# Performance work log

Hardware: AMD Instinct MI355X
Metric: run time of the kernel (lower is better)

## Reference

```python
import jax, jax.numpy as jnp
import numpy as np

B, N, C = 16, 577, 768
H, D = 12, 64
HID = 3072
EPS = 1e-5


def setup_inputs() -> dict:
    key = jax.random.key(0)
    ks = jax.random.split(key, 5)
    s = 0.02
    return {
        "x": jax.random.normal(ks[0], (B, N, C), jnp.float32),
        "w_qkv": jax.random.normal(ks[1], (C, 3 * C), jnp.float32) * s,
        "b_qkv": jnp.zeros((3 * C,), jnp.float32),
        "w_proj": jax.random.normal(ks[2], (C, C), jnp.float32) * s,
        "b_proj": jnp.zeros((C,), jnp.float32),
        "g1": jnp.ones((C,), jnp.float32),
        "be1": jnp.zeros((C,), jnp.float32),
        "g2": jnp.ones((C,), jnp.float32),
        "be2": jnp.zeros((C,), jnp.float32),
        "w1": jax.random.normal(ks[3], (C, HID), jnp.float32) * s,
        "b1": jnp.zeros((HID,), jnp.float32),
        "w2": jax.random.normal(ks[4], (HID, C), jnp.float32) * s,
        "b2": jnp.zeros((C,), jnp.float32),
    }


def _layernorm(x, g, b):
    mu = jnp.mean(x, axis=-1, keepdims=True)
    var = jnp.mean(jnp.square(x - mu), axis=-1, keepdims=True)
    return (x - mu) * jax.lax.rsqrt(var + EPS) * g + b


def reference(x, w_qkv, b_qkv, w_proj, b_proj, g1, be1, g2, be2, w1, b1, w2, b2):
    # --- pre-norm MHA ---
    xn = _layernorm(x, g1, be1)
    qkv = xn @ w_qkv + b_qkv                      # [B,N,3C]
    qkv = qkv.reshape(B, N, 3, H, D).transpose(2, 0, 3, 1, 4)  # [3,B,H,N,D]
    q, k, v = qkv[0], qkv[1], qkv[2]
    scale = 1.0 / jnp.sqrt(jnp.float32(D))
    scores = jnp.einsum("bhnd,bhmd->bhnm", q, k) * scale
    attn_weights = jax.nn.softmax(scores, axis=-1)  # [B,H,N,N]
    ctx = jnp.einsum("bhnm,bhmd->bhnd", attn_weights, v)
    ctx = ctx.transpose(0, 2, 1, 3).reshape(B, N, C)
    attn_out = ctx @ w_proj + b_proj
    x = x + attn_out
    # --- MLP (exact GELU, matching nn.GELU default) ---
    h = _layernorm(x, g2, be2) @ w1 + b1
    h = jax.nn.gelu(h, approximate=False)
    x = x + (h @ w2 + b2)
    return x, attn_weights
```

## Files before the change

### kernel.cpp

```cpp
#include <hip/hip_runtime.h>
#include <hip/hip_bf16.h>
#include <cmath>

constexpr int B_ = 16, N_ = 577, C_ = 768, H_ = 12, D_ = 64, HID_ = 3072;
constexpr int ROWS_ = B_ * N_;
constexpr int BH_ = B_ * H_;
constexpr int KVT_ = 10;
constexpr int QBLK_ = 10;

typedef __attribute__((ext_vector_type(8))) __bf16 bf16x8;
typedef __attribute__((ext_vector_type(4))) float f32x4;
typedef __attribute__((ext_vector_type(4), aligned(4))) float f32x4u;

#define DEVI __device__ __forceinline__

DEVI unsigned short f2bf(float f) {
  unsigned u = __float_as_uint(f);
  return (unsigned short)((u + 0x7fffu + ((u >> 16) & 1u)) >> 16);
}
DEVI float bf2f(unsigned short u) { return __uint_as_float(((unsigned)u) << 16); }

DEVI void gload16(const void* src, void* dst) {
  __builtin_amdgcn_global_load_lds(
      (const __attribute__((address_space(1))) char*)src,
      (__attribute__((address_space(3))) char*)dst, 16, 0, 0);
}
#define VMCNT0 asm volatile("s_waitcnt vmcnt(0)" ::: "memory")
#define VMW(n) asm volatile("s_waitcnt vmcnt(" #n ")" ::: "memory")
#define FENCE asm volatile("" ::: "memory")
#define RAWBAR do { FENCE; __builtin_amdgcn_s_barrier(); FENCE; } while (0)

__global__ __launch_bounds__(256) void cvtT_kernel(const float* __restrict__ in,
                                                   unsigned short* __restrict__ out,
                                                   int K, int N) {
  __shared__ float t[64][65];
  int n0 = blockIdx.x * 64, k0 = blockIdx.y * 64;
  int tx = threadIdx.x & 63, ty = threadIdx.x >> 6;
#pragma unroll
  for (int r = 0; r < 16; r++) {
    int kr = ty * 16 + r;
    t[kr][tx] = in[(long)(k0 + kr) * N + n0 + tx];
  }
  __syncthreads();
#pragma unroll
  for (int r = 0; r < 16; r++) {
    int nr = ty * 16 + r;
    out[(long)(n0 + nr) * K + k0 + tx] = f2bf(t[tx][nr]);
  }
}

__global__ __launch_bounds__(256) void ln_kernel(const float* __restrict__ x,
                                                 const float* __restrict__ g,
                                                 const float* __restrict__ be,
                                                 unsigned short* __restrict__ out) {
  int row = blockIdx.x;
  const float* xr = x + (long)row * C_;
  float v[3];
  float s = 0.f, s2 = 0.f;
#pragma unroll
  for (int j = 0; j < 3; j++) {
    int i = threadIdx.x + j * 256;
    v[j] = xr[i];
    s += v[j];
    s2 += v[j] * v[j];
  }
#pragma unroll
  for (int o = 32; o > 0; o >>= 1) {
    s += __shfl_down(s, o);
    s2 += __shfl_down(s2, o);
  }
  __shared__ float sh[8];
  int w = threadIdx.x >> 6;
  if ((threadIdx.x & 63) == 0) { sh[w] = s; sh[4 + w] = s2; }
  __syncthreads();
  s = sh[0] + sh[1] + sh[2] + sh[3];
  s2 = sh[4] + sh[5] + sh[6] + sh[7];
  float mu = s * (1.f / C_);
  float var = s2 * (1.f / C_) - mu * mu;
  float rs = rsqrtf(var + 1e-5f);
#pragma unroll
  for (int j = 0; j < 3; j++) {
    int i = threadIdx.x + j * 256;
    out[(long)row * C_ + i] = f2bf((v[j] - mu) * rs * g[i] + be[i]);
  }
}

__global__ __launch_bounds__(256) void attn_kernel(
    const unsigned short* __restrict__ qg,
    const unsigned short* __restrict__ kg,
    const unsigned short* __restrict__ vt,
    float* __restrict__ attn,
    unsigned short* __restrict__ ctx) {
  __shared__ unsigned short Ks[3][64][64];
  __shared__ unsigned short Vs[3][64][64];
  __shared__ unsigned short Ps[4][16][72];
  const int wgid = (blockIdx.x & 7) * (BH_ * QBLK_ / 8) + (blockIdx.x >> 3);
  const int bh = wgid / QBLK_, qb = wgid % QBLK_;
  const int b = bh / H_, h = bh % H_;
  const int tid = threadIdx.x, wave = tid >> 6, lane = tid & 63;
  const int l15 = lane & 15, l4 = lane >> 4;
  const int q0w = qb * 64 + wave * 16;

  const unsigned short* Qh = qg + (long)bh * N_ * D_;
  const char* Kb = (const char*)(kg + (long)bh * N_ * D_);
  const char* Vb = (const char*)(vt + (long)bh * D_ * N_);

  int qrc = q0w + l15; if (qrc >= N_) qrc = N_ - 1;
  bf16x8 qa0 = *(const bf16x8*)(Qh + (long)qrc * D_ + l4 * 8);
  bf16x8 qa1 = *(const bf16x8*)(Qh + (long)qrc * D_ + 32 + l4 * 8);

  auto srcAddr = [&](const char* g0, long rstride, int i) -> const char* {
    int off = i * 4096 + tid * 16;
    int row = off >> 7, colD = off & 127;
    return g0 + (long)row * rstride + (colD ^ ((row & 7) << 4));
  };
  auto stageK = [&](int bu, int kt) {
    const char* g0 = Kb + (long)kt * 8192;
#pragma unroll
    for (int i = 0; i < 2; i++)
      gload16(srcAddr(g0, 128, i), ((char*)Ks) + bu * 8192 + i * 4096 + wave * 1024);
  };
  auto stageV = [&](int bu, int kt) {
    const char* g0 = Vb + (long)kt * 128;
#pragma unroll
    for (int i = 0; i < 2; i++)
      gload16(srcAddr(g0, (long)N_ * 2, i), ((char*)Vs) + bu * 8192 + i * 4096 + wave * 1024);
  };
  auto rdK = [&](int bu, int row, int colb) -> bf16x8 {
    return *(const bf16x8*)(((const char*)Ks) + bu * 8192 + row * 128 +
                            (colb ^ ((row & 7) << 4)));
  };
  auto rdV = [&](int bu, int row, int colb) -> bf16x8 {
    return *(const bf16x8*)(((const char*)Vs) + bu * 8192 + row * 128 +
                            (colb ^ ((row & 7) << 4)));
  };
  auto computeS = [&](int bu, int kv0, f32x4 (&s)[4]) {
#pragma unroll
    for (int nf = 0; nf < 4; nf++) {
      int row = nf * 16 + l15;
      bf16x8 k0v = rdK(bu, row, l4 * 16);
      bf16x8 k1v = rdK(bu, row, 64 + l4 * 16);
      f32x4 z = {0.f, 0.f, 0.f, 0.f};
      z = __builtin_amdgcn_mfma_f32_16x16x32_bf16(qa0, k0v, z, 0, 0, 0);
      z = __builtin_amdgcn_mfma_f32_16x16x32_bf16(qa1, k1v, z, 0, 0, 0);
      if (kv0 + row >= N_) z = f32x4{-1e30f, -1e30f, -1e30f, -1e30f};
      s[nf] = z;
    }
  };

  float m_ln[4], l_ln[4];
#pragma unroll
  for (int r = 0; r < 4; r++) { m_ln[r] = -1e30f; l_ln[r] = 0.f; }

  stageK(0, 0); stageK(1, 1);
#pragma unroll
  for (int kt = 0; kt < KVT_; kt++) {
    const int bu = kt % 3;
    if (kt < KVT_ - 1) { VMW(2); } else { VMW(0); }
    RAWBAR;
    if (kt + 2 < KVT_) stageK((kt + 2) % 3, kt + 2);
    f32x4 s[4];
    computeS(bu, kt * 64, s);
#pragma unroll
    for (int r = 0; r < 4; r++) {
      float t0 = fmaxf(fmaxf(s[0][r], s[1][r]), fmaxf(s[2][r], s[3][r]));
      float mn = fmaxf(m_ln[r], t0);
      float sc = __expf(m_ln[r] - mn);
      l_ln[r] = l_ln[r] * sc + __expf(s[0][r] - mn) + __expf(s[1][r] - mn) +
                __expf(s[2][r] - mn) + __expf(s[3][r] - mn);
      m_ln[r] = mn;
    }
  }

  RAWBAR;
  stageK(0, 0); stageV(0, 0); stageK(1, 1); stageV(1, 1);

  float m_run[4], inv_l[4];
#pragma unroll
  for (int r = 0; r < 4; r++) {
    float m = m_ln[r];
#pragma unroll
    for (int o = 1; o < 16; o <<= 1) m = fmaxf(m, __shfl_xor(m, o));
    float li = l_ln[r] * __expf(m_ln[r] - m);
#pragma unroll
    for (int o = 1; o < 16; o <<= 1) li += __shfl_xor(li, o);
    m_run[r] = m;
    inv_l[r] = 1.f / li;
  }

  f32x4 cacc[4];
#pragma unroll
  for (int nf = 0; nf < 4; nf++) cacc[nf] = f32x4{0.f, 0.f, 0.f, 0.f};

#pragma unroll
  for (int kt = 0; kt < KVT_; kt++) {
    const int bu = kt % 3;
    const int kv0 = kt * 64;
    if (kt == 0) { VMW(4); }
    else if (kt == 1) { VMW(8); }
    else if (kt < KVT_ - 1) { VMW(12); }
    else { VMW(8); }
    RAWBAR;
    if (kt + 2 < KVT_) { stageK((kt + 2) % 3, kt + 2); stageV((kt + 2) % 3, kt + 2); }
    f32x4 s[4];
    computeS(bu, kv0, s);
#pragma unroll
    for (int nf = 0; nf < 4; nf++)
#pragma unroll
      for (int r = 0; r < 4; r++) {
        float p = __expf(s[nf][r] - m_run[r]) * inv_l[r];
        Ps[wave][l4 * 4 + r][nf * 16 + l15] = f2bf(p);
      }
    if (kt < KVT_ - 1) {
      int prow = lane >> 4;
      int c0 = (lane & 15) * 4;
#pragma unroll
      for (int rg = 0; rg < 4; rg++) {
        int row = rg * 4 + prow;
        int qv = q0w + row;
        if (qv < N_) {
          ushort4 pb = *(const ushort4*)&Ps[wave][row][c0];
          f32x4u f;
          f[0] = bf2f(pb.x); f[1] = bf2f(pb.y); f[2] = bf2f(pb.z); f[3] = bf2f(pb.w);
          __builtin_nontemporal_store(
              f, (f32x4u*)(attn + ((long)bh * N_ + qv) * N_ + kv0 + c0));
        }
      }
    } else {
      if ((lane & 15) == 0) {
        int prow = lane >> 4;
#pragma unroll
        for (int rg = 0; rg < 4; rg++) {
          int row = rg * 4 + prow;
          int qv = q0w + row;
          if (qv < N_)
            __builtin_nontemporal_store(bf2f(Ps[wave][row][0]),
                                        attn + ((long)bh * N_ + qv) * N_ + 576);
        }
      }
    }
#pragma unroll
    for (int ks = 0; ks < 2; ks++) {
      bf16x8 pa = *(const bf16x8*)&Ps[wave][l15][ks * 32 + l4 * 8];
#pragma unroll
      for (int nf = 0; nf < 4; nf++) {
        bf16x8 vb = rdV(bu, nf * 16 + l15, ks * 64 + l4 * 16);
        cacc[nf] = __builtin_amdgcn_mfma_f32_16x16x32_bf16(pa, vb, cacc[nf], 0, 0, 0);
      }
    }
  }

#pragma unroll
  for (int nf = 0; nf < 4; nf++)
#pragma unroll
    for (int r = 0; r < 4; r++) {
      int qv = q0w + l4 * 4 + r;
      if (qv >= N_) continue;
      int d = nf * 16 + l15;
      ctx[((long)b * N_ + qv) * C_ + h * D_ + d] = f2bf(cacc[nf][r]);
    }
}

template <int EPI>
__global__ __launch_bounds__(256) void gemm128(
    const unsigned short* __restrict__ A,
    const unsigned short* __restrict__ BT,
    int M, int K, int Nc,
    void* __restrict__ outp, const float* __restrict__ bias,
    const float* __restrict__ resid) {
  __shared__ unsigned short As[2][128][64];
  __shared__ unsigned short Bs[2][128][64];
  const int tid = threadIdx.x, wave = tid >> 6, lane = tid & 63;
  const int l15 = lane & 15, l4 = lane >> 4;
  const long m0 = (long)blockIdx.y * 128, n0 = (long)blockIdx.x * 128;
  const int wr = (wave >> 1) * 64, wc = (wave & 1) * 64;

  f32x4 acc[4][4];
#pragma unroll
  for (int i = 0; i < 4; i++)
#pragma unroll
    for (int j = 0; j < 4; j++) acc[i][j] = f32x4{0.f, 0.f, 0.f, 0.f};

  auto stageA = [&](int buf, int t) {
#pragma unroll
    for (int i = 0; i < 4; i++) {
      int off = i * 4096 + tid * 16;
      int row = off >> 7, colD = off & 127;
      long gr = m0 + row; if (gr >= M) gr = M - 1;
      const char* src = (const char*)A + (gr * (long)K + (long)t * 64) * 2 +
                        (colD ^ ((row & 7) << 4));
      char* dst = ((char*)As) + buf * 16384 + i * 4096 + wave * 1024;
      gload16(src, dst);
    }
  };
  auto stageB = [&](int buf, int t) {
#pragma unroll
    for (int i = 0; i < 4; i++) {
      int off = i * 4096 + tid * 16;
      int row = off >> 7, colD = off & 127;
      const char* src = (const char*)BT + ((n0 + row) * (long)K + (long)t * 64) * 2 +
                        (colD ^ ((row & 7) << 4));
      char* dst = ((char*)Bs) + buf * 16384 + i * 4096 + wave * 1024;
      gload16(src, dst);
    }
  };

  const int nt = K / 64;
  stageA(0, 0); stageB(0, 0);
  VMCNT0; __syncthreads();
  int buf = 0;
  for (int t = 0; t < nt; t++) {
    if (t + 1 < nt) { stageA(buf ^ 1, t + 1); stageB(buf ^ 1, t + 1); }
    bf16x8 af[4][2], bfr[4][2];
#pragma unroll
    for (int mf = 0; mf < 4; mf++)
#pragma unroll
      for (int kk = 0; kk < 2; kk++) {
        int row = wr + mf * 16 + l15, colb = kk * 64 + l4 * 16;
        af[mf][kk] = *(const bf16x8*)(((const char*)As) + buf * 16384 + row * 128 +
                                      (colb ^ ((row & 7) << 4)));
      }
#pragma unroll
    for (int nf = 0; nf < 4; nf++)
#pragma unroll
      for (int kk = 0; kk < 2; kk++) {
        int row = wc + nf * 16 + l15, colb = kk * 64 + l4 * 16;
        bfr[nf][kk] = *(const bf16x8*)(((const char*)Bs) + buf * 16384 + row * 128 +
                                       (colb ^ ((row & 7) << 4)));
      }
#pragma unroll
    for (int kk = 0; kk < 2; kk++)
#pragma unroll
      for (int mf = 0; mf < 4; mf++)
#pragma unroll
        for (int nf = 0; nf < 4; nf++)
          acc[mf][nf] =
              __builtin_amdgcn_mfma_f32_16x16x32_bf16(af[mf][kk], bfr[nf][kk], acc[mf][nf], 0, 0, 0);
    VMCNT0; __syncthreads();
    buf ^= 1;
  }

#pragma unroll
  for (int mf = 0; mf < 4; mf++)
#pragma unroll
    for (int nf = 0; nf < 4; nf++)
#pragma unroll
      for (int r = 0; r < 4; r++) {
        long row = m0 + wr + mf * 16 + l4 * 4 + r;
        long col = n0 + wc + nf * 16 + l15;
        if (row >= M) continue;
        float v = acc[mf][nf][r];
        if constexpr (EPI == 3 || EPI == 5) {
          float* o = (float*)outp;
          long idx = row * (long)Nc + col;
          o[idx] = v + bias[col] + resid[idx];
        } else if constexpr (EPI == 4) {
          v += bias[col];
          float ge = 0.5f * v * (1.f + erff(v * 0.70710678118654752f));
          ((unsigned short*)outp)[row * (long)Nc + col] = f2bf(ge);
        }
      }
}

template <int EPI>
__global__ __launch_bounds__(512, 2) void gemm256(
    const unsigned short* __restrict__ A,
    const unsigned short* __restrict__ BT,
    int M, int K, int Nc,
    void* __restrict__ outp, const float* __restrict__ bias,
    const float* __restrict__ resid) {
  __shared__ unsigned short smem[2][2][2][128][64];
  const int tid = threadIdx.x, wave = tid >> 6, lane = tid & 63;
  const int l15 = lane & 15, l4 = lane >> 4;
  const int wm = wave >> 2, wn = wave & 3;

  const int nbx = gridDim.x;
  const int nwg = nbx * gridDim.y;
  int orig = blockIdx.y * nbx + blockIdx.x;
  int qq = nwg >> 3, r8 = nwg & 7;
  int xcd = orig & 7, idx = orig >> 3;
  int wg = (xcd < r8 ? xcd * (qq + 1) : r8 * (qq + 1) + (xcd - r8) * qq) + idx;
  const long m0 = (long)(wg / nbx) * 256;
  const long n0 = (long)(wg % nbx) * 256;

  f32x4 acc[2][2][4][2];
#pragma unroll
  for (int a = 0; a < 2; a++)
#pragma unroll
    for (int b = 0; b < 2; b++)
#pragma unroll
      for (int m = 0; m < 4; m++)
#pragma unroll
        for (int n = 0; n < 2; n++) acc[a][b][m][n] = f32x4{0.f, 0.f, 0.f, 0.f};

  auto stage = [&](int d, int op, int half, int t) {
#pragma unroll
    for (int it = 0; it < 2; it++) {
      int off = it * 8192 + tid * 16;
      int lrow = off >> 7, colb = off & 127;
      long grow;
      if (op == 0) {
        grow = m0 + half * 128 + lrow;
        if (grow >= M) grow = M - 1;
      } else {
        grow = n0 + half * 128 + lrow;
      }
      const unsigned short* gp = (op == 0) ? A : BT;
      const char* src = (const char*)(gp + grow * (long)K + (long)t * 64) +
                        (colb ^ ((lrow & 7) << 4));
      char* dst = ((char*)smem) + (((d * 2 + op) * 2 + half) * 16384) + off;
      gload16(src, dst);
    }
  };
  auto rdfrag = [&](int d, int op, int half, int lr, int kk) -> bf16x8 {
    const char* p = ((const char*)smem) + (((d * 2 + op) * 2 + half) * 16384) + lr * 128 +
                    ((kk * 64 + l4 * 16) ^ ((lr & 7) << 4));
    return *(const bf16x8*)p;
  };

  bf16x8 av[4][2];

#define PHASE(d, qm, qn, STAGECODE, VMCODE)                                              \
  {                                                                                      \
    if constexpr (qn == 0) {                                                             \
      _Pragma("unroll") for (int m = 0; m < 4; m++)                                      \
          _Pragma("unroll") for (int kk = 0; kk < 2; kk++)                               \
              av[m][kk] = rdfrag(d, 0, qm, wm * 64 + m * 16 + l15, kk);                  \
    }                                                                                    \
    bf16x8 bv[2][2];                                                                     \
    _Pragma("unroll") for (int n = 0; n < 2; n++)                                        \
        _Pragma("unroll") for (int kk = 0; kk < 2; kk++)                                 \
            bv[n][kk] = rdfrag(d, 1, qn, wn * 32 + n * 16 + l15, kk);                    \
    STAGECODE;                                                                           \
    VMCODE;                                                                              \
    RAWBAR;                                                                              \
    __builtin_amdgcn_s_setprio(1);                                                       \
    _Pragma("unroll") for (int kk = 0; kk < 2; kk++)                                     \
        _Pragma("unroll") for (int m = 0; m < 4; m++)                                    \
            _Pragma("unroll") for (int n = 0; n < 2; n++)                                \
                acc[qm][qn][m][n] = __builtin_amdgcn_mfma_f32_16x16x32_bf16(             \
                    av[m][kk], bv[n][kk], acc[qm][qn][m][n], 0, 0, 0);                   \
    __builtin_amdgcn_s_setprio(0);                                                       \
    RAWBAR;                                                                              \
  }

  const int nt = K / 64, ni = nt / 2;
  stage(0, 0, 0, 0); stage(0, 0, 1, 0); stage(0, 1, 0, 0); stage(0, 1, 1, 0);
  stage(1, 0, 0, 1); stage(1, 0, 1, 1); stage(1, 1, 0, 1); stage(1, 1, 1, 1);
  asm volatile("s_waitcnt vmcnt(8)" ::: "memory");
  RAWBAR;

  for (int i = 0; i < ni; i++) {
    const int t1 = 2 * i + 1, t2 = 2 * i + 2, t3 = 2 * i + 3;
    PHASE(0, 0, 0, { if (i > 0) stage(1, 0, 1, t1); }, {});
    PHASE(0, 0, 1, { if (i > 0) stage(1, 1, 1, t1); }, {});
    PHASE(0, 1, 0, { if (t2 < nt) stage(0, 0, 0, t2); }, {});
    PHASE(0, 1, 1, { if (t2 < nt) stage(0, 1, 0, t2); },
          { if (t2 < nt) { asm volatile("s_waitcnt vmcnt(4)" ::: "memory"); }
            else { asm volatile("s_waitcnt vmcnt(0)" ::: "memory"); } });
    PHASE(1, 0, 0, { if (t2 < nt) stage(0, 0, 1, t2); }, {});
    PHASE(1, 0, 1, { if (t2 < nt) stage(0, 1, 1, t2); }, {});
    PHASE(1, 1, 0, { if (t3 < nt) stage(1, 0, 0, t3); }, {});
    PHASE(1, 1, 1, { if (t3 < nt) stage(1, 1, 0, t3); },
          { if (t3 < nt) { asm volatile("s_waitcnt vmcnt(4)" ::: "memory"); }
            else { asm volatile("s_waitcnt vmcnt(0)" ::: "memory"); } });
  }
#undef PHASE

#pragma unroll
  for (int qm = 0; qm < 2; qm++)
#pragma unroll
    for (int qn = 0; qn < 2; qn++)
#pragma unroll
      for (int m = 0; m < 4; m++)
#pragma unroll
        for (int n = 0; n < 2; n++)
#pragma unroll
          for (int r = 0; r < 4; r++) {
            long row = m0 + qm * 128 + wm * 64 + m * 16 + l4 * 4 + r;
            long col = n0 + qn * 128 + wn * 32 + n * 16 + l15;
            if (row >= M) continue;
            float v = acc[qm][qn][m][n][r];
            if constexpr (EPI == 0) {
              v += bias[col];
              int which = (int)col / C_;
              int rem = (int)col % C_;
              int hh = rem >> 6, d = rem & 63;
              int bb = (int)row / N_, nn = (int)row % N_;
              if (which == 0) v *= 0.125f;
              unsigned short* o = (unsigned short*)outp;
              long base = (long)which * ((long)BH_ * N_ * D_);
              long oidx;
              if (which < 2)
                oidx = base + (((long)(bb * H_ + hh)) * N_ + nn) * D_ + d;
              else
                oidx = base + (((long)(bb * H_ + hh)) * D_ + d) * N_ + nn;
              o[oidx] = f2bf(v);
            } else if constexpr (EPI == 4) {
              v += bias[col];
              float ge = 0.5f * v * (1.f + erff(v * 0.70710678118654752f));
              ((unsigned short*)outp)[row * (long)Nc + col] = f2bf(ge);
            } else {
              float* o = (float*)outp;
              long oidx = row * (long)Nc + col;
              o[oidx] = v + bias[col] + resid[oidx];
            }
          }
}

extern "C" void kernel_launch(void* const* d_in, const int* in_sizes, int n_in,
                              void* d_out, int out_size, void* d_ws, size_t ws_size,
                              hipStream_t stream) {
  const float* x = (const float*)d_in[0];
  const float* w_qkv = (const float*)d_in[1];
  const float* b_qkv = (const float*)d_in[2];
  const float* w_proj = (const float*)d_in[3];
  const float* b_proj = (const float*)d_in[4];
  const float* g1 = (const float*)d_in[5];
  const float* be1 = (const float*)d_in[6];
  const float* g2 = (const float*)d_in[7];
  const float* be2 = (const float*)d_in[8];
  const float* w1 = (const float*)d_in[9];
  const float* b1 = (const float*)d_in[10];
  const float* w2 = (const float*)d_in[11];
  const float* b2 = (const float*)d_in[12];

  char* ws = (char*)d_ws;
  const size_t SZ_TOK_BF = (size_t)ROWS_ * C_ * 2;
  unsigned short* xn = (unsigned short*)(ws);
  unsigned short* q = (unsigned short*)(ws + SZ_TOK_BF);
  unsigned short* v = (unsigned short*)(ws + 3 * SZ_TOK_BF);
  unsigned short* ctx = (unsigned short*)(ws + 4 * SZ_TOK_BF);
  unsigned short* hbuf = q;
  float* x1 = (float*)(ws + 5 * SZ_TOK_BF);
  unsigned short* wqkvT = (unsigned short*)(ws + 5 * SZ_TOK_BF + (size_t)ROWS_ * C_ * 4);
  unsigned short* wprojT = wqkvT + (size_t)C_ * 3 * C_;
  unsigned short* w1T = wprojT + (size_t)C_ * C_;
  unsigned short* w2T = w1T + (size_t)C_ * HID_;

  float* out_x = (float*)d_out;
  float* attn = out_x + (size_t)ROWS_ * C_;

  cvtT_kernel<<<dim3(3 * C_ / 64, C_ / 64), 256, 0, stream>>>(w_qkv, wqkvT, C_, 3 * C_);
  cvtT_kernel<<<dim3(C_ / 64, C_ / 64), 256, 0, stream>>>(w_proj, wprojT, C_, C_);
  cvtT_kernel<<<dim3(HID_ / 64, C_ / 64), 256, 0, stream>>>(w1, w1T, C_, HID_);
  cvtT_kernel<<<dim3(C_ / 64, HID_ / 64), 256, 0, stream>>>(w2, w2T, HID_, C_);

  ln_kernel<<<ROWS_, 256, 0, stream>>>(x, g1, be1, xn);

  {
    dim3 g(3 * C_ / 256, (ROWS_ + 255) / 256);
    gemm256<0><<<g, 512, 0, stream>>>(xn, wqkvT, ROWS_, C_, 3 * C_, q, b_qkv, nullptr);
  }
  attn_kernel<<<BH_ * QBLK_, 256, 0, stream>>>(q, q + (size_t)BH_ * N_ * D_, v, attn, ctx);
  {
    dim3 g(C_ / 128, (ROWS_ + 127) / 128);
    gemm128<3><<<g, 256, 0, stream>>>(ctx, wprojT, ROWS_, C_, C_, x1, b_proj, x);
  }
  ln_kernel<<<ROWS_, 256, 0, stream>>>(x1, g2, be2, xn);
  {
    dim3 g(HID_ / 256, (ROWS_ + 255) / 256);
    gemm256<4><<<g, 512, 0, stream>>>(xn, w1T, ROWS_, C_, HID_, hbuf, b1, nullptr);
  }
  {
    dim3 g(C_ / 128, (ROWS_ + 127) / 128);
    gemm128<5><<<g, 256, 0, stream>>>(hbuf, w2T, ROWS_, HID_, C_, out_x, b2, x1);
  }
}
```

Before: 484.2 us.

## Transpose attention score MFMA so each lane owns a query row, store probabilities directly

The attention kernel swaps the MFMA operand order so each lane holds scores for a single query row across key columns. Row max and sum then become per-lane scalars with two cross-lane shuffles instead of per-row arrays reduced over 16 lanes. Attention weights are written straight from registers as fp32 instead of round-tripping through shared memory as bf16, and out-of-range query rows are redirected to a dump buffer rather than branched around. K/V staging drops from triple to double buffering with full vmcnt waits, which shrinks LDS use but risks exposing load latency.

New measurement: 491.2 us. About the same (+1.4%).

```diff
diff --git a/kernel.cpp b/kernel.cpp
--- a/kernel.cpp
+++ b/kernel.cpp
@@ -18,7 +18,6 @@
   unsigned u = __float_as_uint(f);
   return (unsigned short)((u + 0x7fffu + ((u >> 16) & 1u)) >> 16);
 }
-DEVI float bf2f(unsigned short u) { return __uint_as_float(((unsigned)u) << 16); }
 
 DEVI void gload16(const void* src, void* dst) {
   __builtin_amdgcn_global_load_lds(
@@ -90,10 +89,11 @@
     const unsigned short* __restrict__ kg,
     const unsigned short* __restrict__ vt,
     float* __restrict__ attn,
-    unsigned short* __restrict__ ctx) {
-  __shared__ unsigned short Ks[3][64][64];
-  __shared__ unsigned short Vs[3][64][64];
-  __shared__ unsigned short Ps[4][16][72];
+    unsigned short* __restrict__ ctx,
+    float* __restrict__ dump) {
+  __shared__ unsigned short Ks[2][64][64];
+  __shared__ unsigned short Vs[2][64][64];
+  __shared__ unsigned short Ps[4][16][40];
   const int wgid = (blockIdx.x & 7) * (BH_ * QBLK_ / 8) + (blockIdx.x >> 3);
   const int bh = wgid / QBLK_, qb = wgid % QBLK_;
   const int b = bh / H_, h = bh % H_;
@@ -134,110 +134,107 @@
     return *(const bf16x8*)(((const char*)Vs) + bu * 8192 + row * 128 +
                             (colb ^ ((row & 7) << 4)));
   };
-  auto computeS = [&](int bu, int kv0, f32x4 (&s)[4]) {
+  auto computeS = [&](int bu, f32x4 (&s)[4]) {
 #pragma unroll
     for (int nf = 0; nf < 4; nf++) {
       int row = nf * 16 + l15;
       bf16x8 k0v = rdK(bu, row, l4 * 16);
       bf16x8 k1v = rdK(bu, row, 64 + l4 * 16);
       f32x4 z = {0.f, 0.f, 0.f, 0.f};
-      z = __builtin_amdgcn_mfma_f32_16x16x32_bf16(qa0, k0v, z, 0, 0, 0);
-      z = __builtin_amdgcn_mfma_f32_16x16x32_bf16(qa1, k1v, z, 0, 0, 0);
-      if (kv0 + row >= N_) z = f32x4{-1e30f, -1e30f, -1e30f, -1e30f};
+      z = __builtin_amdgcn_mfma_f32_16x16x32_bf16(k0v, qa0, z, 0, 0, 0);
+      z = __builtin_amdgcn_mfma_f32_16x16x32_bf16(k1v, qa1, z, 0, 0, 0);
       s[nf] = z;
     }
   };
-
-  float m_ln[4], l_ln[4];
-#pragma unroll
-  for (int r = 0; r < 4; r++) { m_ln[r] = -1e30f; l_ln[r] = 0.f; }
-
-  stageK(0, 0); stageK(1, 1);
+  auto maskLast = [&](f32x4 (&s)[4]) {
+#pragma unroll
+    for (int nf = 0; nf < 4; nf++)
+#pragma unroll
+      for (int r = 0; r < 4; r++) {
+        if (nf == 0 && r == 0)
+          s[nf][r] = (l4 == 0) ? s[nf][r] : -1e30f;
+        else
+          s[nf][r] = -1e30f;
+      }
+  };
+
+  float m_ln = -1e30f, l_ln = 0.f;
+  stageK(0, 0);
 #pragma unroll
   for (int kt = 0; kt < KVT_; kt++) {
-    const int bu = kt % 3;
-    if (kt < KVT_ - 1) { VMW(2); } else { VMW(0); }
+    VMCNT0; RAWBAR;
+    if (kt + 1 < KVT_) stageK((kt + 1) & 1, kt + 1);
+    f32x4 s[4];
+    computeS(kt & 1, s);
+    if (kt == KVT_ - 1) maskLast(s);
+    float mt = s[0][0];
+#pragma unroll
+    for (int nf = 0; nf < 4; nf++)
+#pragma unroll
+      for (int r = 0; r < 4; r++) mt = fmaxf(mt, s[nf][r]);
+    float mn = fmaxf(m_ln, mt);
+    float acc = 0.f;
+#pragma unroll
+    for (int nf = 0; nf < 4; nf++)
+#pragma unroll
+      for (int r = 0; r < 4; r++) acc += __expf(s[nf][r] - mn);
+    l_ln = l_ln * __expf(m_ln - mn) + acc;
+    m_ln = mn;
+  }
+
+  RAWBAR;
+  stageK(0, 0); stageV(0, 0);
+
+  float m = fmaxf(m_ln, __shfl_xor(m_ln, 16));
+  m = fmaxf(m, __shfl_xor(m, 32));
+  float lr = l_ln * __expf(m_ln - m);
+  lr += __shfl_xor(lr, 16);
+  lr += __shfl_xor(lr, 32);
+  float inv_l = 1.f / lr;
+
+  f32x4 cacc[4];
+#pragma unroll
+  for (int nf = 0; nf < 4; nf++) cacc[nf] = f32x4{0.f, 0.f, 0.f, 0.f};
+
+  const int qv = q0w + l15;
+  const bool qok = qv < N_;
+  float* prow = attn + ((long)bh * N_ + (qok ? qv : 0)) * N_;
+
+#pragma unroll
+  for (int kt = 0; kt < KVT_; kt++) {
+    const int bu = kt & 1;
+    if (kt == 0) { VMW(0); } else { VMW(4); }
     RAWBAR;
-    if (kt + 2 < KVT_) stageK((kt + 2) % 3, kt + 2);
+    if (kt + 1 < KVT_) { stageK((kt + 1) & 1, kt + 1); stageV((kt + 1) & 1, kt + 1); }
     f32x4 s[4];
-    computeS(bu, kt * 64, s);
-#pragma unroll
-    for (int r = 0; r < 4; r++) {
-      float t0 = fmaxf(fmaxf(s[0][r], s[1][r]), fmaxf(s[2][r], s[3][r]));
-      float mn = fmaxf(m_ln[r], t0);
-      float sc = __expf(m_ln[r] - mn);
-      l_ln[r] = l_ln[r] * sc + __expf(s[0][r] - mn) + __expf(s[1][r] - mn) +
-                __expf(s[2][r] - mn) + __expf(s[3][r] - mn);
-      m_ln[r] = mn;
-    }
-  }
-
-  RAWBAR;
-  stageK(0, 0); stageV(0, 0); stageK(1, 1); stageV(1, 1);
-
-  float m_run[4], inv_l[4];
-#pragma unroll
-  for (int r = 0; r < 4; r++) {
-    float m = m_ln[r];
-#pragma unroll
-    for (int o = 1; o < 16; o <<= 1) m = fmaxf(m, __shfl_xor(m, o));
-    float li = l_ln[r] * __expf(m_ln[r] - m);
-#pragma unroll
-    for (int o = 1; o < 16; o <<= 1) li += __shfl_xor(li, o);
-    m_run[r] = m;
-    inv_l[r] = 1.f / li;
-  }
-
-  f32x4 cacc[4];
-#pragma unroll
-  for (int nf = 0; nf < 4; nf++) cacc[nf] = f32x4{0.f, 0.f, 0.f, 0.f};
-
-#pragma unroll
-  for (int kt = 0; kt < KVT_; kt++) {
-    const int bu = kt % 3;
-    const int kv0 = kt * 64;
-    if (kt == 0) { VMW(4); }
-    else if (kt == 1) { VMW(8); }
-    else if (kt < KVT_ - 1) { VMW(12); }
-    else { VMW(8); }
-    RAWBAR;
-    if (kt + 2 < KVT_) { stageK((kt + 2) % 3, kt + 2); stageV((kt + 2) % 3, kt + 2); }
-    f32x4 s[4];
-    computeS(bu, kv0, s);
+    computeS(bu, s);
+    if (kt == KVT_ - 1) maskLast(s);
+    float p[4][4];
 #pragma unroll
     for (int nf = 0; nf < 4; nf++)
 #pragma unroll
-      for (int r = 0; r < 4; r++) {
-        float p = __expf(s[nf][r] - m_run[r]) * inv_l[r];
-        Ps[wave][l4 * 4 + r][nf * 16 + l15] = f2bf(p);
-      }
+      for (int r = 0; r < 4; r++) p[nf][r] = __expf(s[nf][r] - m) * inv_l;
+
     if (kt < KVT_ - 1) {
-      int prow = lane >> 4;
-      int c0 = (lane & 15) * 4;
-#pragma unroll
-      for (int rg = 0; rg < 4; rg++) {
-        int row = rg * 4 + prow;
-        int qv = q0w + row;
-        if (qv < N_) {
-          ushort4 pb = *(const ushort4*)&Ps[wave][row][c0];
-          f32x4u f;
-          f[0] = bf2f(pb.x); f[1] = bf2f(pb.y); f[2] = bf2f(pb.z); f[3] = bf2f(pb.w);
-          __builtin_nontemporal_store(
-              f, (f32x4u*)(attn + ((long)bh * N_ + qv) * N_ + kv0 + c0));
-        }
+#pragma unroll
+      for (int nf = 0; nf < 4; nf++) {
+        f32x4u val;
+        val[0] = p[nf][0]; val[1] = p[nf][1]; val[2] = p[nf][2]; val[3] = p[nf][3];
+        float* a = qok ? (prow + kt * 64 + nf * 16 + l4 * 4) : (dump + tid * 4);
+        *(f32x4u*)a = val;
       }
     } else {
-      if ((lane & 15) == 0) {
-        int prow = lane >> 4;
-#pragma unroll
-        for (int rg = 0; rg < 4; rg++) {
-          int row = rg * 4 + prow;
-          int qv = q0w + row;
-          if (qv < N_)
-            __builtin_nontemporal_store(bf2f(Ps[wave][row][0]),
-                                        attn + ((long)bh * N_ + qv) * N_ + 576);
-        }
-      }
+      float* a = (qok && l4 == 0) ? (prow + 576) : (dump + tid);
+      *a = p[0][0];
+    }
+
+#pragma unroll
+    for (int nf = 0; nf < 4; nf++) {
+      unsigned lo = (__float_as_uint(p[nf][1]) & 0xffff0000u) |
+                    (__float_as_uint(p[nf][0]) >> 16);
+      unsigned hi = (__float_as_uint(p[nf][3]) & 0xffff0000u) |
+                    (__float_as_uint(p[nf][2]) >> 16);
+      *(uint2*)&Ps[wave][l15][nf * 16 + l4 * 4] = uint2{lo, hi};
     }
 #pragma unroll
     for (int ks = 0; ks < 2; ks++) {
@@ -254,10 +251,10 @@
   for (int nf = 0; nf < 4; nf++)
 #pragma unroll
     for (int r = 0; r < 4; r++) {
-      int qv = q0w + l4 * 4 + r;
-      if (qv >= N_) continue;
+      int qw = q0w + l4 * 4 + r;
+      if (qw >= N_) continue;
       int d = nf * 16 + l15;
-      ctx[((long)b * N_ + qv) * C_ + h * D_ + d] = f2bf(cacc[nf][r]);
+      ctx[((long)b * N_ + qw) * C_ + h * D_ + d] = f2bf(cacc[nf][r]);
     }
 }
 
@@ -537,6 +534,7 @@
   unsigned short* wprojT = wqkvT + (size_t)C_ * 3 * C_;
   unsigned short* w1T = wprojT + (size_t)C_ * C_;
   unsigned short* w2T = w1T + (size_t)C_ * HID_;
+  float* dump = (float*)(w2T + (size_t)HID_ * C_);
 
   float* out_x = (float*)d_out;
   float* attn = out_x + (size_t)ROWS_ * C_;
@@ -552,7 +550,8 @@
     dim3 g(3 * C_ / 256, (ROWS_ + 255) / 256);
     gemm256<0><<<g, 512, 0, stream>>>(xn, wqkvT, ROWS_, C_, 3 * C_, q, b_qkv, nullptr);
   }
-  attn_kernel<<<BH_ * QBLK_, 256, 0, stream>>>(q, q + (size_t)BH_ * N_ * D_, v, attn, ctx);
+  attn_kernel<<<BH_ * QBLK_, 256, 0, stream>>>(q, q + (size_t)BH_ * N_ * D_, v, attn, ctx,
+                                               dump);
   {
     dim3 g(C_ / 128, (ROWS_ + 127) / 128);
     gemm128<3><<<g, 256, 0, stream>>>(ctx, wprojT, ROWS_, C_, C_, x1, b_proj, x);
```
